# Kernel optimization log

Measured on AMD Instinct MI355X. Metric: run time of the kernel, lower is better.

Reference implementation:

```python
import jax, jax.numpy as jnp
import numpy as np

D_MOD = 256; H = 8; DH = 32; L_MAX = 96; NUM_MODULES = 15; NUM_TASKS = 7; LN_EPS = 1e-5


def _ln(x, s, b):
    mu = x.mean(-1, keepdims=True)
    v = ((x - mu) ** 2).mean(-1, keepdims=True)
    return (x - mu) * jax.lax.rsqrt(v + LN_EPS) * s + b


def _mha(x, w, b, key_mask, bias):
    # w: [4, D, D] (q,k,v,o), b: [4, D]
    B_, S, _ = x.shape
    q = (x @ w[0] + b[0]).reshape(B_, S, H, DH)
    k = (x @ w[1] + b[1]).reshape(B_, S, H, DH)
    v = (x @ w[2] + b[2]).reshape(B_, S, H, DH)
    logits = jnp.einsum('bihd,bjhd->bhij', q, k) / np.sqrt(DH).astype(np.float32)
    if bias is not None:
        logits = logits + bias
    if key_mask is not None:
        logits = jnp.where(key_mask[:, None, None, :], -1e9, logits)
    a = jax.nn.softmax(logits, axis=-1)
    o = jnp.einsum('bhij,bjhd->bihd', a, v).reshape(B_, S, D_MOD)
    return o @ w[3] + b[3]


def setup_inputs() -> dict:
    key = jax.random.key(0)
    ks = iter(jax.random.split(key, 48))
    B = 64
    M = B * NUM_MODULES  # 960 modules
    lengths = (16 + (np.arange(M) % 81)).astype(np.int32)  # ragged, max 96
    N = int(lengths.sum())  # 53346
    batch_ids = jnp.asarray(np.repeat(np.arange(M), lengths), jnp.int32)
    feats = jax.random.normal(next(ks), (N, D_MOD), jnp.float32)
    coords = jax.random.uniform(next(ks), (N, 3), jnp.float32) * 10.0
    module_to_event = jnp.asarray(np.arange(M) // NUM_MODULES, jnp.int32)
    module_pos = jnp.asarray(np.arange(M) % NUM_MODULES, jnp.int32)
    x_glob = jax.random.normal(next(ks), (B, 16), jnp.float32)

    def nrm(shape):
        return jax.random.normal(next(ks), shape, jnp.float32) * 0.02

    params = dict(
        cls_mod=nrm((1, 1, D_MOD)),
        empty_mod_emb=nrm((D_MOD,)),
        cls_task=nrm((1, NUM_TASKS, D_MOD)),
        pos_emb_table=nrm((1 + NUM_MODULES, D_MOD)),
        mod_attn_w=nrm((2, 4, D_MOD, D_MOD)), mod_attn_b=jnp.zeros((2, 4, D_MOD)),
        mod_rel=nrm((2, H, 3)),
        mod_ln_s=jnp.ones((2, 2, D_MOD)), mod_ln_b=jnp.zeros((2, 2, D_MOD)),
        mod_ffn_w1=nrm((2, D_MOD, 4 * D_MOD)), mod_ffn_b1=jnp.zeros((2, 4 * D_MOD)),
        mod_ffn_w2=nrm((2, 4 * D_MOD, D_MOD)), mod_ffn_b2=jnp.zeros((2, D_MOD)),
        glob_w1=nrm((16, D_MOD)), glob_b1=jnp.zeros((D_MOD,)),
        glob_w2=nrm((D_MOD, D_MOD)), glob_b2=jnp.zeros((D_MOD,)),
        evt_attn_w=nrm((3, 4, D_MOD, D_MOD)), evt_attn_b=jnp.zeros((3, 4, D_MOD)),
        evt_ln_s=jnp.ones((3, 2, D_MOD)), evt_ln_b=jnp.zeros((3, 2, D_MOD)),
        evt_ffn_w1=nrm((3, D_MOD, 2048)), evt_ffn_b1=jnp.zeros((3, 2048)),
        evt_ffn_w2=nrm((3, 2048, D_MOD)), evt_ffn_b2=jnp.zeros((3, D_MOD)),
        head_w=nrm((D_MOD, 16)), head_b=jnp.zeros((16,)),
    )
    return dict(feats=feats, coords=coords, batch_ids=batch_ids,
                module_to_event=module_to_event, module_pos=module_pos,
                x_glob=x_glob, **params)


def reference(feats, coords, batch_ids, module_to_event, module_pos, x_glob,
              cls_mod, empty_mod_emb, cls_task, pos_emb_table,
              mod_attn_w, mod_attn_b, mod_rel, mod_ln_s, mod_ln_b,
              mod_ffn_w1, mod_ffn_b1, mod_ffn_w2, mod_ffn_b2,
              glob_w1, glob_b1, glob_w2, glob_b2,
              evt_attn_w, evt_attn_b, evt_ln_s, evt_ln_b,
              evt_ffn_w1, evt_ffn_b1, evt_ffn_w2, evt_ffn_b2,
              head_w, head_b):
    M = module_to_event.shape[0]
    N = feats.shape[0]
    B = x_glob.shape[0]
    # --- ragged group/pad (pad_sequence over per-module masks) ---
    counts = jax.ops.segment_sum(jnp.ones((N,), jnp.int32), batch_ids, num_segments=M)
    starts = jnp.cumsum(counts) - counts
    pos = jnp.arange(N, dtype=jnp.int32) - starts[batch_ids]  # within-module rank (batch_ids sorted)
    pf = jnp.zeros((M, L_MAX, D_MOD), feats.dtype).at[batch_ids, pos].set(feats)
    pc = jnp.zeros((M, L_MAX, 3), coords.dtype).at[batch_ids, pos].set(coords)
    pad_mask = jnp.arange(L_MAX)[None, :] >= counts[:, None]
    # --- module transformer with relative-position bias, CLS token prepended ---
    seq = jnp.concatenate([jnp.broadcast_to(cls_mod, (M, 1, D_MOD)), pf], axis=1)  # [M,97,256]
    km = jnp.concatenate([jnp.zeros((M, 1), bool), pad_mask], axis=1)
    sc = jnp.concatenate([jnp.zeros((M, 1, 3), coords.dtype), pc], axis=1)
    rel = sc[:, :, None, :] - sc[:, None, :, :]  # [M,S,S,3]
    for l in range(2):
        bias = jnp.einsum('mijc,hc->mhij', rel, mod_rel[l])
        seq = _ln(seq + _mha(seq, mod_attn_w[l], mod_attn_b[l], km, bias), mod_ln_s[l, 0], mod_ln_b[l, 0])
        ff = jax.nn.gelu(seq @ mod_ffn_w1[l] + mod_ffn_b1[l], approximate=False) @ mod_ffn_w2[l] + mod_ffn_b2[l]
        seq = _ln(seq + ff, mod_ln_s[l, 1], mod_ln_b[l, 1])
    mod_emb = seq[:, 0]  # [M,256]
    # --- scatter-assembly into dense per-event tensor ---
    pad_evt = jnp.tile(empty_mod_emb[None, None, :], (B, NUM_MODULES, 1))
    pad_evt = pad_evt.at[module_to_event, module_pos].set(mod_emb)
    glob = (jax.nn.gelu(x_glob @ glob_w1 + glob_b1, approximate=False) @ glob_w2 + glob_b2)[:, None, :]
    se = jnp.concatenate([jnp.broadcast_to(cls_task, (B, NUM_TASKS, D_MOD)), glob, pad_evt], axis=1)  # [B,23,256]
    se = se.at[:, NUM_TASKS:].add(pos_emb_table[None])
    # --- event transformer (post-norm, ReLU FFN d_ff=2048, 3 layers) ---
    for l in range(3):
        se = _ln(se + _mha(se, evt_attn_w[l], evt_attn_b[l], None, None), evt_ln_s[l, 0], evt_ln_b[l, 0])
        ff = jax.nn.relu(se @ evt_ffn_w1[l] + evt_ffn_b1[l]) @ evt_ffn_w2[l] + evt_ffn_b2[l]
        se = _ln(se + ff, evt_ln_s[l, 1], evt_ln_b[l, 1])
    emb = se[:, :NUM_TASKS]

    def head(tok, sl):
        return emb[:, tok] @ head_w[:, sl] + head_b[sl]

    def norml(x):
        return x / jnp.maximum(jnp.linalg.norm(x, axis=-1, keepdims=True), 1e-12)

    sp = jax.nn.softplus
    # order: flavour(4), charm(1), e_vis_cc, e_vis_nc, pt_miss, lep_mag, lep_dir(3), jet_mag, jet_dir(3)
    # NOTE: original code's if/else overwrites flavour/charm with softplus too (replicated).
    out = jnp.concatenate([
        sp(head(0, slice(0, 4))), sp(head(1, slice(4, 5))), sp(head(2, slice(5, 6))),
        sp(head(3, slice(6, 7))), sp(head(4, slice(7, 8))), sp(head(5, slice(8, 9))),
        norml(head(5, slice(9, 12))), sp(head(6, slice(12, 13))), norml(head(6, slice(13, 16)))
    ], axis=-1)  # [B,16]
    return out
```

## Files before the change

### kernel.cpp

```cpp
#include <hip/hip_runtime.h>
#include <hip/hip_bf16.h>
#include <math.h>

typedef unsigned short u16;
typedef unsigned int u32;
typedef __bf16 bf16v8 __attribute__((ext_vector_type(8)));
typedef _Float16 f16v8 __attribute__((ext_vector_type(8)));
typedef __attribute__((ext_vector_type(4))) float f32x4;

#define D_MOD 256
#define NHEAD 8
#define DHEAD 32
#define SEQL 97
#define NTOKE 23

__device__ __forceinline__ float bf2f(u16 u){
  union { unsigned int i; float f; } x; x.i = ((unsigned int)u) << 16; return x.f;
}
__device__ __forceinline__ u16 f2bf(float f){
  return __builtin_bit_cast(u16, (__bf16)f);
}
__device__ __forceinline__ float gelu_fast(float v){
  float z = v * 0.70710678118654752f;
  float az = fabsf(z);
  float t = __builtin_amdgcn_rcpf(fmaf(0.3275911f, az, 1.0f));
  float p = t*(0.254829592f + t*(-0.284496736f + t*(1.421413741f + t*(-1.453152027f + t*1.061405429f))));
  float e = __expf(-z*z);
  float y = 1.0f - p*e;
  float erfz = copysignf(y, z);
  return 0.5f * v * (1.0f + erfz);
}
__device__ __forceinline__ void gld16(const void* g, void* l){
  __builtin_amdgcn_global_load_lds((const __attribute__((address_space(1))) void*)g,
                                   (__attribute__((address_space(3))) void*)l, 16, 0, 0);
}

__global__ __launch_bounds__(256) void prep_all(
    const float* __restrict__ aw, const float* __restrict__ ew,
    const float* __restrict__ f1m, const float* __restrict__ f2m,
    const float* __restrict__ f1e, const float* __restrict__ f2e,
    const float* __restrict__ gw2,
    u16* __restrict__ modWT, u16* __restrict__ evtWT,
    u16* __restrict__ modF1T, u16* __restrict__ modF2T,
    u16* __restrict__ evtF1T, u16* __restrict__ evtF2T,
    u16* __restrict__ globW2T,
    u16* __restrict__ WP, u16* __restrict__ F1P, u16* __restrict__ F2P)
{
  const int id = blockIdx.x;
  const float* src; u16* dst; u16* pk = nullptr; int K, N, kx, nx, t; long sS, dS;
  if (id < 512)      { t = id;        src = aw;  dst = modWT;   K=256;  N=256;  kx=8;  nx=8;  sS=65536;  dS=65536;  }
  else if (id < 1280){ t = id - 512;  src = ew;  dst = evtWT;   K=256;  N=256;  kx=8;  nx=8;  sS=65536;  dS=65536;  pk = WP;  }
  else if (id < 1792){ t = id - 1280; src = f1m; dst = modF1T;  K=256;  N=1024; kx=8;  nx=32; sS=262144; dS=262144; }
  else if (id < 2304){ t = id - 1792; src = f2m; dst = modF2T;  K=1024; N=256;  kx=32; nx=8;  sS=262144; dS=262144; }
  else if (id < 3840){ t = id - 2304; src = f1e; dst = evtF1T;  K=256;  N=2048; kx=8;  nx=64; sS=524288; dS=524288; pk = F1P; }
  else if (id < 5376){ t = id - 3840; src = f2e; dst = evtF2T;  K=2048; N=256;  kx=64; nx=8;  sS=524288; dS=524288; pk = F2P; }
  else               { t = id - 5376; src = gw2; dst = globW2T; K=256;  N=256;  kx=8;  nx=8;  sS=65536;  dS=65536;  }
  const int per = kx * nx;
  const int z = t / per, rem = t % per;
  const int k0 = (rem % kx) * 32, n0 = (rem / kx) * 32;
  src += (long)z * sS; dst += (long)z * dS;
  __shared__ float tt[32][33];
  const int tx = threadIdx.x & 31, ty = threadIdx.x >> 5;
  #pragma unroll
  for (int r = ty; r < 32; r += 8)
    tt[r][tx] = src[(long)(k0 + r) * N + n0 + tx];
  __syncthreads();
  #pragma unroll
  for (int r = ty; r < 32; r += 8)
    dst[(long)(n0 + r) * K + k0 + tx] = f2bf(tt[tx][r]);
  if (pk && threadIdx.x < 128){
    const int q = threadIdx.x >> 6, l = threadIdx.x & 63;
    const int nb = (n0 >> 4) + q, kb = k0 >> 5;
    const int c = q*16 + (l & 15);
    const int klb = (l >> 4) * 8;
    const long fragi = (long)nb * (K/32) + kb;
    u16 frag[8];
    #pragma unroll
    for (int e = 0; e < 8; e++) frag[e] = f2bf(tt[klb + e][c]);
    u16* d = pk + (long)z * (long)N * K + (fragi*64 + l)*8;
    *(uint4*)d = *(const uint4*)frag;
  }
}

__global__ void count_k(const int* __restrict__ bids, int* __restrict__ counts, int n){
  int i = blockIdx.x * blockDim.x + threadIdx.x;
  if (i < n) atomicAdd(&counts[bids[i]], 1);
}

__global__ void scan_k(const int* __restrict__ counts, int* __restrict__ starts, int M){
  __shared__ int buf[1024];
  int t = threadIdx.x;
  int v = (t < M) ? counts[t] : 0;
  buf[t] = v;
  __syncthreads();
  for (int o = 1; o < 1024; o <<= 1){
    int x = (t >= o) ? buf[t - o] : 0;
    __syncthreads();
    buf[t] += x;
    __syncthreads();
  }
  if (t < M) starts[t] = buf[t] - v;
}

__global__ __launch_bounds__(64) void cls_fill(u16* __restrict__ seqc, const float* __restrict__ cls_mod,
                                               const int* __restrict__ starts){
  int m = blockIdx.x, t = threadIdx.x;
  long row = (long)starts[m] + m;
  const float4 v = *(const float4*)(cls_mod + t * 4);
  u16* d = seqc + row * D_MOD + t * 4;
  d[0] = f2bf(v.x); d[1] = f2bf(v.y); d[2] = f2bf(v.z); d[3] = f2bf(v.w);
}

__global__ __launch_bounds__(64) void scatter_k(const float* __restrict__ feats, const float* __restrict__ coords,
                          const int* __restrict__ bids, u16* __restrict__ seqc, float* __restrict__ scc){
  int i = blockIdx.x, t = threadIdx.x;
  long row = (long)i + bids[i] + 1;
  const float4 v = *(const float4*)(feats + (long)i * D_MOD + t * 4);
  u16* d = seqc + row * D_MOD + t * 4;
  d[0] = f2bf(v.x); d[1] = f2bf(v.y); d[2] = f2bf(v.z); d[3] = f2bf(v.w);
  if (t < 3) scc[row * 3 + t] = coords[(long)i * 3 + t];
}

template<int EPI>
__global__ __launch_bounds__(512) void gemm256(
    const u16* __restrict__ A, const u16* __restrict__ Wt,
    const float* __restrict__ bias, const u16* __restrict__ resid,
    u16* __restrict__ C, int K, int N)
{
  __shared__ char smemraw[49152];
  u16* As = (u16*)smemraw;
  u16* Bs = (u16*)(smemraw + 32768);
  float* stg = (float*)smemraw;

  const int tid = threadIdx.x;
  const int w = tid >> 6, l = tid & 63;
  const int wr = w >> 1, wc = w & 1;

  const long nwg = (long)gridDim.x * gridDim.y;
  const long orig = (long)blockIdx.y * gridDim.x + blockIdx.x;
  const long q = nwg >> 3, r = nwg & 7;
  const long xcd = orig & 7, idx = orig >> 3;
  const long swz = (xcd < r ? xcd * (q + 1) : r * (q + 1) + (xcd - r) * q) + idx;
  const int colb = (int)(swz % gridDim.x);
  const long rowb = swz / gridDim.x;
  const long row0 = rowb * 256;
  const int col0 = colb * 128;

  const int fr = l & 15;
  const int ko = (l >> 4) * 8;
  f32x4 acc[4][4] = {};

  for (int kt = 0; kt < K; kt += 64){
    __syncthreads();
    #pragma unroll
    for (int p = 0; p < 4; p++){
      const int s = p * 512 + tid;
      const int inner = s & 1023, half = s >> 10;
      gld16(A + (row0 + (inner >> 2)) * K + kt + half*32 + (inner & 3)*8,
            As + (p*512 + w*64) * 8);
    }
    #pragma unroll
    for (int p = 0; p < 2; p++){
      const int s = p * 512 + tid;
      const int inner = s & 511, half = s >> 9;
      gld16(Wt + (long)(col0 + (inner >> 2)) * K + kt + half*32 + (inner & 3)*8,
            Bs + (p*512 + w*64) * 8);
    }
    __syncthreads();
    #pragma unroll
    for (int kk2 = 0; kk2 < 2; kk2++){
      bf16v8 af[4], bfv[4];
      #pragma unroll
      for (int mi = 0; mi < 4; mi++)
        af[mi] = __builtin_bit_cast(bf16v8, *(const uint4*)(As + kk2*8192 + (wr*64 + mi*16 + fr)*32 + ko));
      #pragma unroll
      for (int ni = 0; ni < 4; ni++)
        bfv[ni] = __builtin_bit_cast(bf16v8, *(const uint4*)(Bs + kk2*4096 + (wc*64 + ni*16 + fr)*32 + ko));
      #pragma unroll
      for (int mi = 0; mi < 4; mi++)
        #pragma unroll
        for (int ni = 0; ni < 4; ni++)
          acc[mi][ni] = __builtin_amdgcn_mfma_f32_16x16x32_bf16(af[mi], bfv[ni], acc[mi][ni], 0, 0, 0);
    }
  }

  const int rq = (l >> 4) * 4;
  #pragma unroll
  for (int p = 0; p < 8; p++){
    __syncthreads();
    if (wr == (p >> 1)){
      #pragma unroll
      for (int mm = 0; mm < 2; mm++){
        const int mi = (p & 1) * 2 + mm;
        #pragma unroll
        for (int ni = 0; ni < 4; ni++){
          const int coll = wc*64 + ni*16 + fr;
          const float bb = bias[col0 + coll];
          #pragma unroll
          for (int j = 0; j < 4; j++){
            float v = acc[mi][ni][j] + bb;
            if (EPI == 1) v = gelu_fast(v);
            if (EPI == 2) v = fmaxf(v, 0.0f);
            stg[(mm*16 + rq + j) * 132 + coll] = v;
          }
        }
      }
    }
    __syncthreads();
    {
      const int rowl = tid >> 4;
      const int cs = (tid & 15) * 8;
      const long gbase = (row0 + p*32 + rowl) * (long)N + col0 + cs;
      float4 lo = *(const float4*)(stg + rowl*132 + cs);
      float4 hi = *(const float4*)(stg + rowl*132 + cs + 4);
      float vv[8] = {lo.x, lo.y, lo.z, lo.w, hi.x, hi.y, hi.z, hi.w};
      if (EPI == 3){
        uint4 rv = *(const uint4*)(resid + gbase);
        const u16* rp = (const u16*)&rv;
        #pragma unroll
        for (int e = 0; e < 8; e++) vv[e] += bf2f(rp[e]);
      }
      uint4 ov;
      u16* op = (u16*)&ov;
      #pragma unroll
      for (int e = 0; e < 8; e++) op[e] = f2bf(vv[e]);
      *(uint4*)(C + gbase) = ov;
    }
  }
}

template<int NT>
__device__ __forceinline__ void attn_body(
    char* __restrict__ smemRaw,
    const u16* __restrict__ qkv, const float* __restrict__ scc,
    const float* __restrict__ rel, const int S, const long base,
    u16* __restrict__ out)
{
  constexpr int KS  = (NT + 1) / 2;
  constexpr int NK  = NT * 16;
  constexpr int STR = (KS * 32 <= 64) ? 64 : 128;
  constexpr int PBYTES = (NK * STR * 2 > NK * 132) ? NK * STR * 2 : NK * 132;
  u16* Pb = (u16*)smemRaw;
  u16* Vt = (u16*)(smemRaw + PBYTES);
  float* pj = (float*)(smemRaw + PBYTES + 32 * STR * 2);

  const int h = blockIdx.y;
  const int tid = threadIdx.x, w = tid >> 6, l = tid & 63;
  const int fr = l & 15, ko = (l >> 4) * 8;

  if (tid < NK){
    float v = 1e30f;
    if (tid < S){
      const float* s3 = scc + (base + tid) * 3;
      v = s3[0]*rel[h*3] + s3[1]*rel[h*3+1] + s3[2]*rel[h*3+2];
    }
    pj[tid] = v;
  }
  for (int idx = tid; idx < NK*32; idx += 256){
    int key = idx >> 5, d = idx & 31;
    float v = bf2f(qkv[(base + key)*768 + 512 + h*32 + d]);
    v = fminf(fmaxf(v, -60000.0f), 60000.0f);
    _Float16 hv = (_Float16)v;
    Vt[d*STR + (key ^ ((d & 7) << 3))] = __builtin_bit_cast(u16, hv);
  }
  for (int idx = tid; idx < 32*16; idx += 256){
    int d = idx >> 4, c = NK + (idx & 15);
    Vt[d*STR + (c ^ ((d & 7) << 3))] = 0;
  }
  for (int idx = tid; idx < NK*16; idx += 256){
    int row = idx >> 4, c = NK + (idx & 15);
    Pb[row*STR + (c ^ ((row & 7) << 3))] = 0;
  }
  __syncthreads();

  f32x4 accs[2][NT];
  bf16v8 kf[NT];
  #pragma unroll
  for (int nt = 0; nt < NT; nt++)
    kf[nt] = __builtin_bit_cast(bf16v8, *(const uint4*)(qkv + (base + nt*16 + fr)*768 + 256 + h*32 + ko));
  #pragma unroll
  for (int rr2 = 0; rr2 < 2; rr2++){
    const int rt = w + rr2*4;
    if (rt > NT - 1) break;
    bf16v8 qf = __builtin_bit_cast(bf16v8, *(const uint4*)(qkv + (base + rt*16 + fr)*768 + h*32 + ko));
    #pragma unroll
    for (int nt = 0; nt < NT; nt++){
      f32x4 z = {0.f, 0.f, 0.f, 0.f};
      accs[rr2][nt] = __builtin_amdgcn_mfma_f32_16x16x32_bf16(qf, kf[nt], z, 0, 0, 0);
    }
  }

  float pjr[NT];
  #pragma unroll
  for (int nt = 0; nt < NT; nt++) pjr[nt] = pj[nt*16 + fr];
  const float SCALE = 0.17677669529663687f;
  #pragma unroll
  for (int rr2 = 0; rr2 < 2; rr2++){
    const int rt = w + rr2*4;
    if (rt > NT - 1) break;
    #pragma unroll
    for (int j = 0; j < 4; j++){
      float x[NT], mx = -1e30f;
      #pragma unroll
      for (int nt = 0; nt < NT; nt++){
        x[nt] = accs[rr2][nt][j] * SCALE - pjr[nt];
        mx = fmaxf(mx, x[nt]);
      }
      #pragma unroll
      for (int o = 1; o < 16; o <<= 1) mx = fmaxf(mx, __shfl_xor(mx, o));
      float sum = 0.f;
      #pragma unroll
      for (int nt = 0; nt < NT; nt++){
        x[nt] = __expf(x[nt] - mx);
        sum += x[nt];
      }
      #pragma unroll
      for (int o = 1; o < 16; o <<= 1) sum += __shfl_xor(sum, o);
      const float inv = 1.0f / sum;
      const int row = rt*16 + (l >> 4)*4 + j;
      #pragma unroll
      for (int nt = 0; nt < NT; nt++){
        _Float16 hp = (_Float16)(x[nt] * inv);
        Pb[row*STR + ((nt*16 + fr) ^ ((row & 7) << 3))] = __builtin_bit_cast(u16, hp);
      }
    }
  }
  __syncthreads();

  f32x4 accO[2][2];
  #pragma unroll
  for (int rr2 = 0; rr2 < 2; rr2++){
    const int rt = w + rr2*4;
    if (rt > NT - 1) break;
    #pragma unroll
    for (int nt = 0; nt < 2; nt++){
      f32x4 z = {0.f, 0.f, 0.f, 0.f};
      accO[rr2][nt] = z;
    }
    #pragma unroll
    for (int ks = 0; ks < KS; ks++){
      const int prow = rt*16 + fr;
      f16v8 pa = __builtin_bit_cast(f16v8, *(const uint4*)(Pb + prow*STR + ((ks*32 + ko) ^ ((prow & 7) << 3))));
      #pragma unroll
      for (int nt = 0; nt < 2; nt++){
        const int vrow = nt*16 + fr;
        f16v8 vb = __builtin_bit_cast(f16v8, *(const uint4*)(Vt + vrow*STR + ((ks*32 + ko) ^ ((vrow & 7) << 3))));
        accO[rr2][nt] = __builtin_amdgcn_mfma_f32_16x16x32_f16(pa, vb, accO[rr2][nt], 0, 0, 0);
      }
    }
  }
  __syncthreads();

  float* O = (float*)smemRaw;
  #pragma unroll
  for (int rr2 = 0; rr2 < 2; rr2++){
    const int rt = w + rr2*4;
    if (rt > NT - 1) break;
    #pragma unroll
    for (int nt = 0; nt < 2; nt++)
      #pragma unroll
      for (int j = 0; j < 4; j++)
        O[(rt*16 + (l>>4)*4 + j)*33 + nt*16 + fr] = accO[rr2][nt][j];
  }
  __syncthreads();
  for (int idx = tid; idx < NK*16; idx += 256){
    const int row = idx >> 4;
    if (row >= S) continue;
    const int c = (idx & 15) * 2;
    const float f0 = O[row*33 + c], f1 = O[row*33 + c + 1];
    u32 pk = (u32)f2bf(f0) | ((u32)f2bf(f1) << 16);
    *(u32*)(out + (base + row)*256 + h*32 + c) = pk;
  }
}

__global__ __launch_bounds__(256) void mod_attn_all(
    const u16* __restrict__ qkv, const float* __restrict__ scc,
    const float* __restrict__ rel, const int* __restrict__ counts,
    const int* __restrict__ starts, u16* __restrict__ out)
{
  __shared__ __align__(16) char smem[37376];
  const int m = blockIdx.x;
  const int S = counts[m] + 1;
  const long base = (long)starts[m] + m;
  if (S <= 48)      attn_body<3>(smem, qkv, scc, rel, S, base, out);
  else if (S <= 80) attn_body<5>(smem, qkv, scc, rel, S, base, out);
  else              attn_body<7>(smem, qkv, scc, rel, S, base, out);
}

__global__ __launch_bounds__(256) void ln_k(u16* __restrict__ x, const float* __restrict__ s,
                                            const float* __restrict__ b, long nrows){
  const long row = (long)blockIdx.x * 4 + (threadIdx.x >> 6);
  if (row >= nrows) return;
  const int t = threadIdx.x & 63;
  u16* xr = x + row * D_MOD;
  uint2 rv = *(const uint2*)(xr + t * 4);
  float v0 = bf2f((u16)(rv.x & 0xffffu));
  float v1 = bf2f((u16)(rv.x >> 16));
  float v2 = bf2f((u16)(rv.y & 0xffffu));
  float v3 = bf2f((u16)(rv.y >> 16));
  float sum = v0 + v1 + v2 + v3;
  float sq  = v0*v0 + v1*v1 + v2*v2 + v3*v3;
  #pragma unroll
  for (int o = 32; o > 0; o >>= 1){
    sum += __shfl_xor(sum, o, 64);
    sq  += __shfl_xor(sq,  o, 64);
  }
  float mu = sum * (1.0f/256.0f);
  float var = sq * (1.0f/256.0f) - mu*mu;
  float rs = rsqrtf(var + 1e-5f);
  int c = t * 4;
  u16 o0 = f2bf((v0-mu)*rs*s[c+0]+b[c+0]);
  u16 o1 = f2bf((v1-mu)*rs*s[c+1]+b[c+1]);
  u16 o2 = f2bf((v2-mu)*rs*s[c+2]+b[c+2]);
  u16 o3 = f2bf((v3-mu)*rs*s[c+3]+b[c+3]);
  uint2 wv;
  wv.x = (unsigned)o0 | ((unsigned)o1 << 16);
  wv.y = (unsigned)o2 | ((unsigned)o3 << 16);
  *(uint2*)(xr + t * 4) = wv;
}

__global__ __launch_bounds__(512, 1) void evt_fused(
    u16* __restrict__ se,
    const u16* __restrict__ attnWP, const float* __restrict__ attnB,
    const u16* __restrict__ f1P, const float* __restrict__ f1B,
    const u16* __restrict__ f2P, const float* __restrict__ f2B,
    const float* __restrict__ lnS, const float* __restrict__ lnB)
{
  __shared__ u16 X[32*264];
  __shared__ u16 Yb[2*32*264];
  __shared__ u16 Sb[8*32*40];
  __shared__ float st1[32*8], st2[32*8];
  __shared__ float muA[32], rsA[32];

  const int b = blockIdx.x;
  const int tid = threadIdx.x, w = tid >> 6, l = tid & 63;
  const int fr = l & 15, hi4 = (l >> 4) * 4, ko = (l >> 4) * 8;
  const long tb = (long)b * NTOKE;
  u16* Sw = Sb + w * 1280;
  u16* Y = Yb;

  for (int idx = tid; idx < 736; idx += 512){
    const int row = idx >> 5, c8 = (idx & 31) * 8;
    *(uint4*)&X[row*264 + c8] = *(const uint4*)(se + (tb + row)*256 + c8);
  }
  for (int idx = tid; idx < 288; idx += 512){
    const int row = 23 + (idx >> 5), c8 = (idx & 31) * 8;
    uint4 z = {0,0,0,0};
    *(uint4*)&X[row*264 + c8] = z;
  }
  __syncthreads();

  for (int lay = 0; lay < 3; lay++){
    const u16*  WlP = attnWP + (long)lay * 4 * 65536;
    const float* Bl = attnB + lay * 1024;
    const u16*  F1  = f1P + (long)lay * 524288;
    const u16*  F2  = f2P + (long)lay * 524288;

    bf16v8 qf[2], kf[2], pa[2];
    {
      bf16v8 wr_[8][2];
      #pragma unroll
      for (int ks = 0; ks < 8; ks++)
        #pragma unroll
        for (int ct = 0; ct < 2; ct++)
          wr_[ks][ct] = __builtin_bit_cast(bf16v8, *(const uint4*)(WlP + ((w*2+ct)*8 + ks)*512 + l*8));
      f32x4 acc[2][2] = {};
      __builtin_amdgcn_s_setprio(1);
      #pragma unroll
      for (int ks = 0; ks < 8; ks++){
        bf16v8 a0 = __builtin_bit_cast(bf16v8, *(const uint4*)&X[fr*264 + ks*32 + ko]);
        bf16v8 a1 = __builtin_bit_cast(bf16v8, *(const uint4*)&X[(16+fr)*264 + ks*32 + ko]);
        #pragma unroll
        for (int ct = 0; ct < 2; ct++){
          acc[0][ct] = __builtin_amdgcn_mfma_f32_16x16x32_bf16(a0, wr_[ks][ct], acc[0][ct], 0, 0, 0);
          acc[1][ct] = __builtin_amdgcn_mfma_f32_16x16x32_bf16(a1, wr_[ks][ct], acc[1][ct], 0, 0, 0);
        }
      }
      __builtin_amdgcn_s_setprio(0);
      #pragma unroll
      for (int rt = 0; rt < 2; rt++)
        #pragma unroll
        for (int ct = 0; ct < 2; ct++){
          const float bb = Bl[w*32 + ct*16 + fr];
          #pragma unroll
          for (int j = 0; j < 4; j++)
            Sw[(rt*16 + hi4 + j)*40 + ct*16 + fr] = f2bf(acc[rt][ct][j] + bb);
        }
      qf[0] = __builtin_bit_cast(bf16v8, *(const uint4*)&Sw[fr*40 + ko]);
      qf[1] = __builtin_bit_cast(bf16v8, *(const uint4*)&Sw[(16+fr)*40 + ko]);
    }
    {
      bf16v8 wr_[8][2];
      #pragma unroll
      for (int ks = 0; ks < 8; ks++)
        #pragma unroll
        for (int ct = 0; ct < 2; ct++)
          wr_[ks][ct] = __builtin_bit_cast(bf16v8, *(const uint4*)(WlP + 65536 + ((w*2+ct)*8 + ks)*512 + l*8));
      f32x4 acc[2][2] = {};
      __builtin_amdgcn_s_setprio(1);
      #pragma unroll
      for (int ks = 0; ks < 8; ks++){
        bf16v8 a0 = __builtin_bit_cast(bf16v8, *(const uint4*)&X[fr*264 + ks*32 + ko]);
        bf16v8 a1 = __builtin_bit_cast(bf16v8, *(const uint4*)&X[(16+fr)*264 + ks*32 + ko]);
        #pragma unroll
        for (int ct = 0; ct < 2; ct++){
          acc[0][ct] = __builtin_amdgcn_mfma_f32_16x16x32_bf16(a0, wr_[ks][ct], acc[0][ct], 0, 0, 0);
          acc[1][ct] = __builtin_amdgcn_mfma_f32_16x16x32_bf16(a1, wr_[ks][ct], acc[1][ct], 0, 0, 0);
        }
      }
      __builtin_amdgcn_s_setprio(0);
      #pragma unroll
      for (int rt = 0; rt < 2; rt++)
        #pragma unroll
        for (int ct = 0; ct < 2; ct++){
          const float bb = Bl[256 + w*32 + ct*16 + fr];
          #pragma unroll
          for (int j = 0; j < 4; j++)
            Sw[(rt*16 + hi4 + j)*40 + ct*16 + fr] = f2bf(acc[rt][ct][j] + bb);
        }
      kf[0] = __builtin_bit_cast(bf16v8, *(const uint4*)&Sw[fr*40 + ko]);
      kf[1] = __builtin_bit_cast(bf16v8, *(const uint4*)&Sw[(16+fr)*40 + ko]);
    }
    {
      f32x4 accS[2][2];
      #pragma unroll
      for (int rt = 0; rt < 2; rt++)
        #pragma unroll
        for (int nt = 0; nt < 2; nt++){
          f32x4 z = {0.f,0.f,0.f,0.f};
          accS[rt][nt] = __builtin_amdgcn_mfma_f32_16x16x32_bf16(qf[rt], kf[nt], z, 0, 0, 0);
        }
      const float SCALE = 0.17677669529663687f;
      const bool v1 = (fr < 7);
      #pragma unroll
      for (int rt = 0; rt < 2; rt++){
        #pragma unroll
        for (int j = 0; j < 4; j++){
          float x0 = accS[rt][0][j] * SCALE;
          float x1 = v1 ? accS[rt][1][j] * SCALE : -1e30f;
          float mx = fmaxf(x0, x1);
          #pragma unroll
          for (int o = 1; o < 16; o <<= 1) mx = fmaxf(mx, __shfl_xor(mx, o));
          float e0 = __expf(x0 - mx);
          float e1 = v1 ? __expf(x1 - mx) : 0.0f;
          float sum = e0 + e1;
          #pragma unroll
          for (int o = 1; o < 16; o <<= 1) sum += __shfl_xor(sum, o);
          const float inv = 1.0f / sum;
          const int row = rt*16 + hi4 + j;
          Sw[row*40 + fr]      = f2bf(e0 * inv);
          Sw[row*40 + 16 + fr] = f2bf(e1 * inv);
        }
      }
      pa[0] = __builtin_bit_cast(bf16v8, *(const uint4*)&Sw[fr*40 + ko]);
      pa[1] = __builtin_bit_cast(bf16v8, *(const uint4*)&Sw[(16+fr)*40 + ko]);
    }
    {
      bf16v8 wr_[8][2];
      #pragma unroll
      for (int ks = 0; ks < 8; ks++)
        #pragma unroll
        for (int ct = 0; ct < 2; ct++)
          wr_[ks][ct] = __builtin_bit_cast(bf16v8, *(const uint4*)(WlP + 131072 + ((w*2+ct)*8 + ks)*512 + l*8));
      f32x4 acc[2][2] = {};
      __builtin_amdgcn_s_setprio(1);
      #pragma unroll
      for (int ks = 0; ks < 8; ks++){
        bf16v8 a0 = __builtin_bit_cast(bf16v8, *(const uint4*)&X[fr*264 + ks*32 + ko]);
        bf16v8 a1 = __builtin_bit_cast(bf16v8, *(const uint4*)&X[(16+fr)*264 + ks*32 + ko]);
        #pragma unroll
        for (int ct = 0; ct < 2; ct++){
          acc[0][ct] = __builtin_amdgcn_mfma_f32_16x16x32_bf16(a0, wr_[ks][ct], acc[0][ct], 0, 0, 0);
          acc[1][ct] = __builtin_amdgcn_mfma_f32_16x16x32_bf16(a1, wr_[ks][ct], acc[1][ct], 0, 0, 0);
        }
      }
      __builtin_amdgcn_s_setprio(0);
      #pragma unroll
      for (int rt = 0; rt < 2; rt++)
        #pragma unroll
        for (int ct = 0; ct < 2; ct++){
          const float bb = Bl[512 + w*32 + ct*16 + fr];
          u16* dst = &Sw[(ct*16 + fr)*40 + rt*16 + hi4];
          #pragma unroll
          for (int j = 0; j < 4; j++)
            dst[j] = f2bf(acc[rt][ct][j] + bb);
        }
      bf16v8 vb0 = __builtin_bit_cast(bf16v8, *(const uint4*)&Sw[fr*40 + ko]);
      bf16v8 vb1 = __builtin_bit_cast(bf16v8, *(const uint4*)&Sw[(16+fr)*40 + ko]);
      f32x4 accO[2][2];
      #pragma unroll
      for (int rt = 0; rt < 2; rt++){
        f32x4 z = {0.f,0.f,0.f,0.f};
        accO[rt][0] = __builtin_amdgcn_mfma_f32_16x16x32_bf16(pa[rt], vb0, z, 0, 0, 0);
        accO[rt][1] = __builtin_amdgcn_mfma_f32_16x16x32_bf16(pa[rt], vb1, z, 0, 0, 0);
      }
      #pragma unroll
      for (int rt = 0; rt < 2; rt++)
        #pragma unroll
        for (int nt = 0; nt < 2; nt++)
          #pragma unroll
          for (int j = 0; j < 4; j++)
            Y[(rt*16 + hi4 + j)*264 + w*32 + nt*16 + fr] = f2bf(accO[rt][nt][j]);
    }
    __syncthreads();

    {
      bf16v8 wr_[8][2];
      #pragma unroll
      for (int ks = 0; ks < 8; ks++)
        #pragma unroll
        for (int ct = 0; ct < 2; ct++)
          wr_[ks][ct] = __builtin_bit_cast(bf16v8, *(const uint4*)(WlP + 196608 + ((w*2+ct)*8 + ks)*512 + l*8));
      f32x4 acc[2][2] = {};
      __builtin_amdgcn_s_setprio(1);
      #pragma unroll
      for (int ks = 0; ks < 8; ks++){
        bf16v8 a0 = __builtin_bit_cast(bf16v8, *(const uint4*)&Y[fr*264 + ks*32 + ko]);
        bf16v8 a1 = __builtin_bit_cast(bf16v8, *(const uint4*)&Y[(16+fr)*264 + ks*32 + ko]);
        #pragma unroll
        for (int ct = 0; ct < 2; ct++){
          acc[0][ct] = __builtin_amdgcn_mfma_f32_16x16x32_bf16(a0, wr_[ks][ct], acc[0][ct], 0, 0, 0);
          acc[1][ct] = __builtin_amdgcn_mfma_f32_16x16x32_bf16(a1, wr_[ks][ct], acc[1][ct], 0, 0, 0);
        }
      }
      __builtin_amdgcn_s_setprio(0);
      float val[2][2][4];
      #pragma unroll
      for (int ct = 0; ct < 2; ct++){
        const int col = w*32 + ct*16 + fr;
        const float bb = Bl[768 + col];
        #pragma unroll
        for (int rt = 0; rt < 2; rt++)
          #pragma unroll
          for (int j = 0; j < 4; j++)
            val[rt][ct][j] = acc[rt][ct][j] + bb + bf2f(X[(rt*16 + hi4 + j)*264 + col]);
      }
      #pragma unroll
      for (int rt = 0; rt < 2; rt++)
        #pragma unroll
        for (int j = 0; j < 4; j++){
          float s1 = val[rt][0][j] + val[rt][1][j];
          float s2 = val[rt][0][j]*val[rt][0][j] + val[rt][1][j]*val[rt][1][j];
          #pragma unroll
          for (int o = 1; o < 16; o <<= 1){ s1 += __shfl_xor(s1, o); s2 += __shfl_xor(s2, o); }
          if (fr == 0){
            const int row = rt*16 + hi4 + j;
            st1[row*8 + w] = s1; st2[row*8 + w] = s2;
          }
        }
      __syncthreads();
      if (tid < 32){
        float s1 = 0.f, s2 = 0.f;
        #pragma unroll
        for (int k = 0; k < 8; k++){ s1 += st1[tid*8 + k]; s2 += st2[tid*8 + k]; }
        const float mu = s1 * (1.0f/256.0f);
        const float var = s2 * (1.0f/256.0f) - mu*mu;
        muA[tid] = mu; rsA[tid] = rsqrtf(var + 1e-5f);
      }
      __syncthreads();
      #pragma unroll
      for (int ct = 0; ct < 2; ct++){
        const int col = w*32 + ct*16 + fr;
        const float lw = lnS[lay*512 + col], lb = lnB[lay*512 + col];
        #pragma unroll
        for (int rt = 0; rt < 2; rt++)
          #pragma unroll
          for (int j = 0; j < 4; j++){
            const int row = rt*16 + hi4 + j;
            X[row*264 + col] = f2bf((val[rt][ct][j] - muA[row]) * rsA[row] * lw + lb);
          }
      }
      __syncthreads();
    }

    {
      f32x4 acc2[2][2] = {};
      for (int c = 0; c < 8; c++){
        u16* Yc = Yb + (c & 1) * 8448;
        bf16v8 w1r[8][2];
        #pragma unroll
        for (int ks = 0; ks < 8; ks++)
          #pragma unroll
          for (int ct = 0; ct < 2; ct++)
            w1r[ks][ct] = __builtin_bit_cast(bf16v8, *(const uint4*)(F1 + (long)((c*16 + w*2 + ct)*8 + ks)*512 + l*8));
        f32x4 acc1[2][2] = {};
        __builtin_amdgcn_s_setprio(1);
        #pragma unroll
        for (int ks = 0; ks < 8; ks++){
          bf16v8 a0 = __builtin_bit_cast(bf16v8, *(const uint4*)&X[fr*264 + ks*32 + ko]);
          bf16v8 a1 = __builtin_bit_cast(bf16v8, *(const uint4*)&X[(16+fr)*264 + ks*32 + ko]);
          #pragma unroll
          for (int ct = 0; ct < 2; ct++){
            acc1[0][ct] = __builtin_amdgcn_mfma_f32_16x16x32_bf16(a0, w1r[ks][ct], acc1[0][ct], 0, 0, 0);
            acc1[1][ct] = __builtin_amdgcn_mfma_f32_16x16x32_bf16(a1, w1r[ks][ct], acc1[1][ct], 0, 0, 0);
          }
        }
        __builtin_amdgcn_s_setprio(0);
        bf16v8 w2r[8][2];
        #pragma unroll
        for (int ks = 0; ks < 8; ks++)
          #pragma unroll
          for (int ct = 0; ct < 2; ct++)
            w2r[ks][ct] = __builtin_bit_cast(bf16v8, *(const uint4*)(F2 + (long)((w*2+ct)*64 + c*8 + ks)*512 + l*8));
        #pragma unroll
        for (int ct = 0; ct < 2; ct++){
          const float bb = f1B[lay*2048 + c*256 + w*32 + ct*16 + fr];
          #pragma unroll
          for (int rt = 0; rt < 2; rt++)
            #pragma unroll
            for (int j = 0; j < 4; j++)
              Yc[(rt*16 + hi4 + j)*264 + w*32 + ct*16 + fr] = f2bf(fmaxf(acc1[rt][ct][j] + bb, 0.0f));
        }
        __syncthreads();
        __builtin_amdgcn_s_setprio(1);
        #pragma unroll
        for (int ks = 0; ks < 8; ks++){
          bf16v8 a0 = __builtin_bit_cast(bf16v8, *(const uint4*)&Yc[fr*264 + ks*32 + ko]);
          bf16v8 a1 = __builtin_bit_cast(bf16v8, *(const uint4*)&Yc[(16+fr)*264 + ks*32 + ko]);
          #pragma unroll
          for (int ct = 0; ct < 2; ct++){
            acc2[0][ct] = __builtin_amdgcn_mfma_f32_16x16x32_bf16(a0, w2r[ks][ct], acc2[0][ct], 0, 0, 0);
            acc2[1][ct] = __builtin_amdgcn_mfma_f32_16x16x32_bf16(a1, w2r[ks][ct], acc2[1][ct], 0, 0, 0);
          }
        }
        __builtin_amdgcn_s_setprio(0);
      }
      __syncthreads();
      float val[2][2][4];
      #pragma unroll
      for (int ct = 0; ct < 2; ct++){
        const int col = w*32 + ct*16 + fr;
        const float bb = f2B[lay*256 + col];
        #pragma unroll
        for (int rt = 0; rt < 2; rt++)
          #pragma unroll
          for (int j = 0; j < 4; j++)
            val[rt][ct][j] = acc2[rt][ct][j] + bb + bf2f(X[(rt*16 + hi4 + j)*264 + col]);
      }
      #pragma unroll
      for (int rt = 0; rt < 2; rt++)
        #pragma unroll
        for (int j = 0; j < 4; j++){
          float s1 = val[rt][0][j] + val[rt][1][j];
          float s2 = val[rt][0][j]*val[rt][0][j] + val[rt][1][j]*val[rt][1][j];
          #pragma unroll
          for (int o = 1; o < 16; o <<= 1){ s1 += __shfl_xor(s1, o); s2 += __shfl_xor(s2, o); }
          if (fr == 0){
            const int row = rt*16 + hi4 + j;
            st1[row*8 + w] = s1; st2[row*8 + w] = s2;
          }
        }
      __syncthreads();
      if (tid < 32){
        float s1 = 0.f, s2 = 0.f;
        #pragma unroll
        for (int k = 0; k < 8; k++){ s1 += st1[tid*8 + k]; s2 += st2[tid*8 + k]; }
        const float mu = s1 * (1.0f/256.0f);
        const float var = s2 * (1.0f/256.0f) - mu*mu;
        muA[tid] = mu; rsA[tid] = rsqrtf(var + 1e-5f);
      }
      __syncthreads();
      #pragma unroll
      for (int ct = 0; ct < 2; ct++){
        const int col = w*32 + ct*16 + fr;
        const float lw = lnS[lay*512 + 256 + col], lb = lnB[lay*512 + 256 + col];
        #pragma unroll
        for (int rt = 0; rt < 2; rt++)
          #pragma unroll
          for (int j = 0; j < 4; j++){
            const int row = rt*16 + hi4 + j;
            X[row*264 + col] = f2bf((val[rt][ct][j] - muA[row]) * rsA[row] * lw + lb);
          }
      }
      __syncthreads();
    }
  }

  for (int idx = tid; idx < 736; idx += 512){
    const int row = idx >> 5, c8 = (idx & 31) * 8;
    *(uint4*)(se + (tb + row)*256 + c8) = *(const uint4*)&X[row*264 + c8];
  }
}

__global__ __launch_bounds__(256) void glob1_k(const float* __restrict__ xg, const float* __restrict__ w1,
                                               const float* __restrict__ b1, u16* __restrict__ h){
  int b = blockIdx.x, d = threadIdx.x;
  float s = b1[d];
  #pragma unroll
  for (int k = 0; k < 16; k++) s += xg[b*16 + k] * w1[k*256 + d];
  h[(long)b*256 + d] = f2bf(gelu_fast(s));
}

__global__ __launch_bounds__(64) void fill_se(u16* __restrict__ se, const float* __restrict__ cls_task,
                                              const u16* __restrict__ globo, const float* __restrict__ pos_emb,
                                              const float* __restrict__ empty_emb){
  int bt = blockIdx.x;
  int b = bt / NTOKE, tk = bt % NTOKE;
  int t = threadIdx.x;
  u16* d = se + (long)bt * D_MOD;
  #pragma unroll
  for (int j = 0; j < 4; j++){
    int c = t*4 + j;
    float v;
    if (tk < 7) v = cls_task[tk*D_MOD + c];
    else if (tk == 7) v = bf2f(globo[(long)b*D_MOD + c]) + pos_emb[c];
    else v = empty_emb[c] + pos_emb[(tk - 7)*D_MOD + c];
    d[c] = f2bf(v);
  }
}

__global__ __launch_bounds__(64) void scatter_mod(u16* __restrict__ se, const u16* __restrict__ seqc,
                                                  const int* __restrict__ m2e, const int* __restrict__ mpos,
                                                  const int* __restrict__ starts,
                                                  const float* __restrict__ pos_emb){
  int m = blockIdx.x, t = threadIdx.x;
  int e = m2e[m], p = mpos[m];
  const u16* src = seqc + ((long)starts[m] + m) * D_MOD;
  u16* dst = se + ((long)e * NTOKE + 8 + p) * D_MOD;
  const float* pe = pos_emb + (long)(1 + p) * D_MOD;
  #pragma unroll
  for (int j = 0; j < 4; j++){
    int c = t*4 + j;
    dst[c] = f2bf(bf2f(src[c]) + pe[c]);
  }
}

__global__ __launch_bounds__(64) void heads_k(const u16* __restrict__ se, const float* __restrict__ hw,
                                              const float* __restrict__ hb, float* __restrict__ out){
  int b = blockIdx.x, t = threadIdx.x;
  __shared__ float raw[16];
  if (t < 16){
    int tok = (t < 4) ? 0 : (t <= 8) ? (t - 3) : (t <= 11) ? 5 : 6;
    const u16* e = se + ((long)b * NTOKE + tok) * D_MOD;
    float s = hb[t];
    for (int d = 0; d < 256; d++) s += bf2f(e[d]) * hw[d*16 + t];
    raw[t] = s;
  }
  __syncthreads();
  if (t < 16){
    float v = raw[t];
    float r;
    if (t <= 8 || t == 12){
      r = fmaxf(v, 0.0f) + log1pf(__expf(-fabsf(v)));
    } else if (t <= 11){
      float n = sqrtf(raw[9]*raw[9] + raw[10]*raw[10] + raw[11]*raw[11]);
      r = v / fmaxf(n, 1e-12f);
    } else {
      float n = sqrtf(raw[13]*raw[13] + raw[14]*raw[14] + raw[15]*raw[15]);
      r = v / fmaxf(n, 1e-12f);
    }
    out[b*16 + t] = r;
  }
}

extern "C" void kernel_launch(void* const* d_in, const int* in_sizes, int n_in,
                              void* d_out, int out_size, void* d_ws, size_t ws_size,
                              hipStream_t stream){
  const float* feats      = (const float*)d_in[0];
  const float* coords     = (const float*)d_in[1];
  const int*   batch_ids  = (const int*)d_in[2];
  const int*   m2e        = (const int*)d_in[3];
  const int*   mpos       = (const int*)d_in[4];
  const float* x_glob     = (const float*)d_in[5];
  const float* cls_mod    = (const float*)d_in[6];
  const float* empty_emb  = (const float*)d_in[7];
  const float* cls_task   = (const float*)d_in[8];
  const float* pos_emb    = (const float*)d_in[9];
  const float* mod_attn_w = (const float*)d_in[10];
  const float* mod_attn_b = (const float*)d_in[11];
  const float* mod_rel    = (const float*)d_in[12];
  const float* mod_ln_s   = (const float*)d_in[13];
  const float* mod_ln_b   = (const float*)d_in[14];
  const float* mod_ffn_w1 = (const float*)d_in[15];
  const float* mod_ffn_b1 = (const float*)d_in[16];
  const float* mod_ffn_w2 = (const float*)d_in[17];
  const float* mod_ffn_b2 = (const float*)d_in[18];
  const float* glob_w1    = (const float*)d_in[19];
  const float* glob_b1    = (const float*)d_in[20];
  const float* glob_w2    = (const float*)d_in[21];
  const float* glob_b2    = (const float*)d_in[22];
  const float* evt_attn_w = (const float*)d_in[23];
  const float* evt_attn_b = (const float*)d_in[24];
  const float* evt_ln_s   = (const float*)d_in[25];
  const float* evt_ln_b   = (const float*)d_in[26];
  const float* evt_ffn_w1 = (const float*)d_in[27];
  const float* evt_ffn_b1 = (const float*)d_in[28];
  const float* evt_ffn_w2 = (const float*)d_in[29];
  const float* evt_ffn_b2 = (const float*)d_in[30];
  const float* head_w     = (const float*)d_in[31];
  const float* head_b     = (const float*)d_in[32];
  float* out = (float*)d_out;

  const int N = in_sizes[0] / 256;
  const int M = in_sizes[3];
  const int B = in_sizes[5] / 16;
  const long CROWS   = (long)M + N;
  const long CROWS_P = (((CROWS + 255) >> 8) << 8) + 256;
  const long TE  = (long)B * NTOKE;

  char* ws = (char*)d_ws;
  u16* modWT   = (u16*)ws;
  u16* evtWT   = modWT + 8L*65536;
  u16* modF1T  = evtWT + 12L*65536;
  u16* modF2T  = modF1T + 2L*262144;
  u16* evtF1T  = modF2T + 2L*262144;
  u16* evtF2T  = evtF1T + 3L*524288;
  u16* globW2T = evtF2T + 3L*524288;
  size_t off = 11468800;
  int* counts = (int*)(ws + off); off += 16*1024;
  int* starts = (int*)(ws + off); off += 16*1024;
  float* scc  = (float*)(ws + off); off += ((size_t)CROWS_P*12 + 255) & ~(size_t)255;
  u16* seqc   = (u16*)(ws + off); off += (size_t)CROWS_P * D_MOD * 2;
  off = (off + 255) & ~(size_t)255;
  const size_t OFF_BIG = off;
  u16* qkv   = (u16*)(ws + OFF_BIG);
  u16* attno = (u16*)(ws + OFF_BIG + (size_t)CROWS_P*768*2);
  u16* ffh   = (u16*)(ws + OFF_BIG);
  u16* se    = (u16*)(ws + OFF_BIG);
  u16* globh = (u16*)(ws + OFF_BIG + 12*1024*1024);
  u16* globo = (u16*)(ws + OFF_BIG + 13*1024*1024);
  u16* evtWP  = (u16*)(ws + OFF_BIG + 120L*1024*1024);
  u16* evtF1P = evtWP + 12L*65536;
  u16* evtF2P = evtF1P + 3L*524288;

  prep_all<<<5440, 256, 0, stream>>>(mod_attn_w, evt_attn_w, mod_ffn_w1, mod_ffn_w2,
                                     evt_ffn_w1, evt_ffn_w2, glob_w2,
                                     modWT, evtWT, modF1T, modF2T, evtF1T, evtF2T, globW2T,
                                     evtWP, evtF1P, evtF2P);

  hipMemsetAsync(counts, 0, (size_t)M*4, stream);
  hipMemsetAsync(scc, 0, (size_t)CROWS_P*12, stream);
  hipMemsetAsync(seqc + CROWS*D_MOD, 0, (size_t)(CROWS_P - CROWS)*D_MOD*2, stream);
  count_k<<<(N + 255)/256, 256, 0, stream>>>(batch_ids, counts, N);
  scan_k<<<1, 1024, 0, stream>>>(counts, starts, M);
  cls_fill<<<M, 64, 0, stream>>>(seqc, cls_mod, starts);
  scatter_k<<<N, 64, 0, stream>>>(feats, coords, batch_ids, seqc, scc);

  const int RB = (int)(CROWS_P / 256);
  for (int l = 0; l < 2; l++){
    gemm256<0><<<dim3(6, RB), 512, 0, stream>>>(seqc, modWT + (long)l*4*65536,
        mod_attn_b + l*1024, nullptr, qkv, 256, 768);
    mod_attn_all<<<dim3(M, NHEAD), 256, 0, stream>>>(qkv, scc, mod_rel + l*24, counts, starts, attno);
    gemm256<3><<<dim3(2, RB), 512, 0, stream>>>(attno, modWT + ((long)l*4+3)*65536,
        mod_attn_b + l*1024 + 768, seqc, seqc, 256, 256);
    ln_k<<<(int)((CROWS + 3)/4), 256, 0, stream>>>(seqc, mod_ln_s + (l*2)*256, mod_ln_b + (l*2)*256, CROWS);
    gemm256<1><<<dim3(8, RB), 512, 0, stream>>>(seqc, modF1T + (long)l*262144,
        mod_ffn_b1 + l*1024, nullptr, ffh, 256, 1024);
    gemm256<3><<<dim3(2, RB), 512, 0, stream>>>(ffh, modF2T + (long)l*262144,
        mod_ffn_b2 + l*256, seqc, seqc, 1024, 256);
    ln_k<<<(int)((CROWS + 3)/4), 256, 0, stream>>>(seqc, mod_ln_s + (l*2+1)*256, mod_ln_b + (l*2+1)*256, CROWS);
  }

  hipMemsetAsync(globh, 0, 256*256*2, stream);
  glob1_k<<<B, 256, 0, stream>>>(x_glob, glob_w1, glob_b1, globh);
  gemm256<0><<<dim3(2, 1), 512, 0, stream>>>(globh, globW2T, glob_b2, nullptr, globo, 256, 256);
  fill_se<<<(int)TE, 64, 0, stream>>>(se, cls_task, globo, pos_emb, empty_emb);
  scatter_mod<<<M, 64, 0, stream>>>(se, seqc, m2e, mpos, starts, pos_emb);

  evt_fused<<<B, 512, 0, stream>>>(se, evtWP, evt_attn_b, evtF1P, evt_ffn_b1,
                                   evtF2P, evt_ffn_b2, evt_ln_s, evt_ln_b);

  heads_k<<<B, 64, 0, stream>>>(se, head_w, head_b, out);
}
```

Before: 825.1 us.

## Fuse residual add and LayerNorm into full-width output GEMM for module layers

Adds a gemm_ln kernel in which each block computes all 256 output columns for 128 rows, adds bias and residual, and applies LayerNorm in the epilogue. It replaces the gemm256<3> plus separate ln_k pair after attention and after the FFN in both module layers. This removes four LayerNorm launches and one read-modify-write of the sequence buffer per fusion. The cost is fewer, larger blocks (RB2 blocks along rows, one along columns), which may reduce parallelism. Padding rows of attno are now zeroed as well.

```diff
diff --git a/kernel.cpp b/kernel.cpp
--- a/kernel.cpp
+++ b/kernel.cpp
@@ -229,6 +229,123 @@
   }
 }
 
+__global__ __launch_bounds__(512) void gemm_ln(
+    const u16* __restrict__ A, const u16* __restrict__ Wt,
+    const float* __restrict__ bias, const u16* __restrict__ resid,
+    u16* __restrict__ C, int K,
+    const float* __restrict__ lnS, const float* __restrict__ lnB)
+{
+  __shared__ char smemraw[49152];
+  u16* As = (u16*)smemraw;
+  u16* Bs = (u16*)(smemraw + 16384);
+  float* stg = (float*)smemraw;
+
+  const int tid = threadIdx.x;
+  const int w = tid >> 6, l = tid & 63;
+  const int wr = w >> 2, wc = w & 3;
+
+  const long nwg = gridDim.y;
+  const long orig = blockIdx.y;
+  const long q = nwg >> 3, r = nwg & 7;
+  const long xcd = orig & 7, idx = orig >> 3;
+  const long swz = (xcd < r ? xcd * (q + 1) : r * (q + 1) + (xcd - r) * q) + idx;
+  const long row0 = swz * 128;
+
+  const int fr = l & 15;
+  const int ko = (l >> 4) * 8;
+  f32x4 acc[4][4] = {};
+
+  for (int kt = 0; kt < K; kt += 64){
+    __syncthreads();
+    #pragma unroll
+    for (int p = 0; p < 2; p++){
+      const int s = p * 512 + tid;
+      const int inner = s & 511, half = s >> 9;
+      gld16(A + (row0 + (inner >> 2)) * K + kt + half*32 + (inner & 3)*8,
+            As + (p*512 + w*64) * 8);
+    }
+    #pragma unroll
+    for (int p = 0; p < 4; p++){
+      const int s = p * 512 + tid;
+      const int inner = s & 1023, half = s >> 10;
+      gld16(Wt + (long)(inner >> 2) * K + kt + half*32 + (inner & 3)*8,
+            Bs + (p*512 + w*64) * 8);
+    }
+    __syncthreads();
+    #pragma unroll
+    for (int kk2 = 0; kk2 < 2; kk2++){
+      bf16v8 af[4], bfv[4];
+      #pragma unroll
+      for (int mi = 0; mi < 4; mi++)
+        af[mi] = __builtin_bit_cast(bf16v8, *(const uint4*)(As + kk2*4096 + (wr*64 + mi*16 + fr)*32 + ko));
+      #pragma unroll
+      for (int ni = 0; ni < 4; ni++)
+        bfv[ni] = __builtin_bit_cast(bf16v8, *(const uint4*)(Bs + kk2*8192 + (wc*64 + ni*16 + fr)*32 + ko));
+      #pragma unroll
+      for (int mi = 0; mi < 4; mi++)
+        #pragma unroll
+        for (int ni = 0; ni < 4; ni++)
+          acc[mi][ni] = __builtin_amdgcn_mfma_f32_16x16x32_bf16(af[mi], bfv[ni], acc[mi][ni], 0, 0, 0);
+    }
+  }
+
+  const int rq = (l >> 4) * 4;
+  #pragma unroll
+  for (int p = 0; p < 4; p++){
+    __syncthreads();
+    if (wr == (p >> 1)){
+      #pragma unroll
+      for (int mm = 0; mm < 2; mm++){
+        const int mi = (p & 1) * 2 + mm;
+        #pragma unroll
+        for (int ni = 0; ni < 4; ni++){
+          const int coll = wc*64 + ni*16 + fr;
+          const float bb = bias[coll];
+          #pragma unroll
+          for (int j = 0; j < 4; j++)
+            stg[(mm*16 + rq + j) * 260 + coll] = acc[mi][ni][j] + bb;
+        }
+      }
+    }
+    __syncthreads();
+    {
+      const int rowl = tid >> 4;
+      const int c0 = (tid & 15) * 16;
+      const long gbase = (row0 + p*32 + rowl) * 256 + c0;
+      float v[16];
+      uint4 r0 = *(const uint4*)(resid + gbase);
+      uint4 r1 = *(const uint4*)(resid + gbase + 8);
+      const u16* rp0 = (const u16*)&r0;
+      const u16* rp1 = (const u16*)&r1;
+      #pragma unroll
+      for (int e = 0; e < 8; e++){
+        v[e]     = stg[rowl*260 + c0 + e]     + bf2f(rp0[e]);
+        v[8 + e] = stg[rowl*260 + c0 + 8 + e] + bf2f(rp1[e]);
+      }
+      float sum = 0.f, sq = 0.f;
+      #pragma unroll
+      for (int e = 0; e < 16; e++){ sum += v[e]; sq += v[e]*v[e]; }
+      #pragma unroll
+      for (int o = 1; o < 16; o <<= 1){
+        sum += __shfl_xor(sum, o);
+        sq  += __shfl_xor(sq,  o);
+      }
+      const float mu = sum * (1.0f/256.0f);
+      const float var = sq * (1.0f/256.0f) - mu*mu;
+      const float rs = rsqrtf(var + 1e-5f);
+      uint4 o0, o1;
+      u16* op0 = (u16*)&o0; u16* op1 = (u16*)&o1;
+      #pragma unroll
+      for (int e = 0; e < 8; e++){
+        op0[e] = f2bf((v[e]     - mu) * rs * lnS[c0 + e]     + lnB[c0 + e]);
+        op1[e] = f2bf((v[8 + e] - mu) * rs * lnS[c0 + 8 + e] + lnB[c0 + 8 + e]);
+      }
+      *(uint4*)(C + gbase)     = o0;
+      *(uint4*)(C + gbase + 8) = o1;
+    }
+  }
+}
+
 template<int NT>
 __device__ __forceinline__ void attn_body(
     char* __restrict__ smemRaw,
@@ -385,38 +502,6 @@
   if (S <= 48)      attn_body<3>(smem, qkv, scc, rel, S, base, out);
   else if (S <= 80) attn_body<5>(smem, qkv, scc, rel, S, base, out);
   else              attn_body<7>(smem, qkv, scc, rel, S, base, out);
-}
-
-__global__ __launch_bounds__(256) void ln_k(u16* __restrict__ x, const float* __restrict__ s,
-                                            const float* __restrict__ b, long nrows){
-  const long row = (long)blockIdx.x * 4 + (threadIdx.x >> 6);
-  if (row >= nrows) return;
-  const int t = threadIdx.x & 63;
-  u16* xr = x + row * D_MOD;
-  uint2 rv = *(const uint2*)(xr + t * 4);
-  float v0 = bf2f((u16)(rv.x & 0xffffu));
-  float v1 = bf2f((u16)(rv.x >> 16));
-  float v2 = bf2f((u16)(rv.y & 0xffffu));
-  float v3 = bf2f((u16)(rv.y >> 16));
-  float sum = v0 + v1 + v2 + v3;
-  float sq  = v0*v0 + v1*v1 + v2*v2 + v3*v3;
-  #pragma unroll
-  for (int o = 32; o > 0; o >>= 1){
-    sum += __shfl_xor(sum, o, 64);
-    sq  += __shfl_xor(sq,  o, 64);
-  }
-  float mu = sum * (1.0f/256.0f);
-  float var = sq * (1.0f/256.0f) - mu*mu;
-  float rs = rsqrtf(var + 1e-5f);
-  int c = t * 4;
-  u16 o0 = f2bf((v0-mu)*rs*s[c+0]+b[c+0]);
-  u16 o1 = f2bf((v1-mu)*rs*s[c+1]+b[c+1]);
-  u16 o2 = f2bf((v2-mu)*rs*s[c+2]+b[c+2]);
-  u16 o3 = f2bf((v3-mu)*rs*s[c+3]+b[c+3]);
-  uint2 wv;
-  wv.x = (unsigned)o0 | ((unsigned)o1 << 16);
-  wv.y = (unsigned)o2 | ((unsigned)o3 << 16);
-  *(uint2*)(xr + t * 4) = wv;
 }
 
 __global__ __launch_bounds__(512, 1) void evt_fused(
@@ -931,24 +1016,26 @@
   hipMemsetAsync(counts, 0, (size_t)M*4, stream);
   hipMemsetAsync(scc, 0, (size_t)CROWS_P*12, stream);
   hipMemsetAsync(seqc + CROWS*D_MOD, 0, (size_t)(CROWS_P - CROWS)*D_MOD*2, stream);
+  hipMemsetAsync(attno + CROWS*D_MOD, 0, (size_t)(CROWS_P - CROWS)*D_MOD*2, stream);
   count_k<<<(N + 255)/256, 256, 0, stream>>>(batch_ids, counts, N);
   scan_k<<<1, 1024, 0, stream>>>(counts, starts, M);
   cls_fill<<<M, 64, 0, stream>>>(seqc, cls_mod, starts);
   scatter_k<<<N, 64, 0, stream>>>(feats, coords, batch_ids, seqc, scc);
 
   const int RB = (int)(CROWS_P / 256);
+  const int RB2 = (int)(CROWS_P / 128);
   for (int l = 0; l < 2; l++){
     gemm256<0><<<dim3(6, RB), 512, 0, stream>>>(seqc, modWT + (long)l*4*65536,
         mod_attn_b + l*1024, nullptr, qkv, 256, 768);
     mod_attn_all<<<dim3(M, NHEAD), 256, 0, stream>>>(qkv, scc, mod_rel + l*24, counts, starts, attno);
-    gemm256<3><<<dim3(2, RB), 512, 0, stream>>>(attno, modWT + ((long)l*4+3)*65536,
-        mod_attn_b + l*1024 + 768, seqc, seqc, 256, 256);
-    ln_k<<<(int)((CROWS + 3)/4), 256, 0, stream>>>(seqc, mod_ln_s + (l*2)*256, mod_ln_b + (l*2)*256, CROWS);
+    gemm_ln<<<dim3(1, RB2), 512, 0, stream>>>(attno, modWT + ((long)l*4+3)*65536,
+        mod_attn_b + l*1024 + 768, seqc, seqc, 256,
+        mod_ln_s + (l*2)*256, mod_ln_b + (l*2)*256);
     gemm256<1><<<dim3(8, RB), 512, 0, stream>>>(seqc, modF1T + (long)l*262144,
         mod_ffn_b1 + l*1024, nullptr, ffh, 256, 1024);
-    gemm256<3><<<dim3(2, RB), 512, 0, stream>>>(ffh, modF2T + (long)l*262144,
-        mod_ffn_b2 + l*256, seqc, seqc, 1024, 256);
-    ln_k<<<(int)((CROWS + 3)/4), 256, 0, stream>>>(seqc, mod_ln_s + (l*2+1)*256, mod_ln_b + (l*2+1)*256, CROWS);
+    gemm_ln<<<dim3(1, RB2), 512, 0, stream>>>(ffh, modF2T + (long)l*262144,
+        mod_ffn_b2 + l*256, seqc, seqc, 1024,
+        mod_ln_s + (l*2+1)*256, mod_ln_b + (l*2+1)*256);
   }
 
   hipMemsetAsync(globh, 0, 256*256*2, stream);
```

Result: slower. 852.6 us (+3.3%).

## Triple-buffer LDS in gemm256 with async prefetch of next K-slice

Applied to the files above, without the earlier changes.

Restructures the gemm256 main loop from a synchronous 64-wide K tile with two barriers per step into a three-buffer pipeline of 32-wide K slices. The next slice is issued with async global-to-LDS loads, followed by a partial vmcnt wait and a single barrier per step. The goal is to hide global load latency behind MFMA work. In exchange LDS grows to 72KB, which may lower occupancy, and the loop now runs twice as many iterations, each with less MFMA work between barriers.

```diff
diff --git a/kernel.cpp b/kernel.cpp
--- a/kernel.cpp
+++ b/kernel.cpp
@@ -127,9 +127,7 @@
     const float* __restrict__ bias, const u16* __restrict__ resid,
     u16* __restrict__ C, int K, int N)
 {
-  __shared__ char smemraw[49152];
-  u16* As = (u16*)smemraw;
-  u16* Bs = (u16*)(smemraw + 32768);
+  __shared__ __align__(16) char smemraw[73728];
   float* stg = (float*)smemraw;
 
   const int tid = threadIdx.x;
@@ -150,38 +148,55 @@
   const int ko = (l >> 4) * 8;
   f32x4 acc[4][4] = {};
 
-  for (int kt = 0; kt < K; kt += 64){
-    __syncthreads();
+  const int sA1 = 512 + tid;
+  const long arow0 = row0 + (tid >> 2), arow1 = row0 + (sA1 >> 2);
+  const int ac0 = (tid & 3) * 8, ac1 = (sA1 & 3) * 8;
+  const long brow = col0 + (tid >> 2);
+  const int bc0 = (tid & 3) * 8;
+  const int ldsA0 = (0*512 + w*64) * 8;
+  const int ldsA1 = (1*512 + w*64) * 8;
+  const int ldsB0 = (w*64) * 8;
+
+  const int NH = K >> 5;
+
+  {
+    u16* bufA = (u16*)smemraw;
+    u16* bufB = (u16*)(smemraw + 16384);
+    gld16(A  + arow0 * K + ac0, bufA + ldsA0);
+    gld16(A  + arow1 * K + ac1, bufA + ldsA1);
+    gld16(Wt + brow  * K + bc0, bufB + ldsB0);
+  }
+
+  int cb = 0, nb = 1;
+  for (int h = 0; h < NH; h++){
+    if (h + 1 < NH){
+      const int kc = (h + 1) * 32;
+      u16* bufA = (u16*)(smemraw + nb * 24576);
+      u16* bufB = (u16*)(smemraw + nb * 24576 + 16384);
+      gld16(A  + arow0 * K + kc + ac0, bufA + ldsA0);
+      gld16(A  + arow1 * K + kc + ac1, bufA + ldsA1);
+      gld16(Wt + brow  * K + kc + bc0, bufB + ldsB0);
+      asm volatile("s_waitcnt vmcnt(3)" ::: "memory");
+    } else {
+      asm volatile("s_waitcnt vmcnt(0)" ::: "memory");
+    }
+    __builtin_amdgcn_s_barrier();
+    __builtin_amdgcn_sched_barrier(0);
+    const u16* cA = (const u16*)(smemraw + cb * 24576);
+    const u16* cB = (const u16*)(smemraw + cb * 24576 + 16384);
+    bf16v8 af[4], bfv[4];
     #pragma unroll
-    for (int p = 0; p < 4; p++){
-      const int s = p * 512 + tid;
-      const int inner = s & 1023, half = s >> 10;
-      gld16(A + (row0 + (inner >> 2)) * K + kt + half*32 + (inner & 3)*8,
-            As + (p*512 + w*64) * 8);
-    }
+    for (int mi = 0; mi < 4; mi++)
+      af[mi] = __builtin_bit_cast(bf16v8, *(const uint4*)(cA + (wr*64 + mi*16 + fr)*32 + ko));
     #pragma unroll
-    for (int p = 0; p < 2; p++){
-      const int s = p * 512 + tid;
-      const int inner = s & 511, half = s >> 9;
-      gld16(Wt + (long)(col0 + (inner >> 2)) * K + kt + half*32 + (inner & 3)*8,
-            Bs + (p*512 + w*64) * 8);
-    }
-    __syncthreads();
+    for (int ni = 0; ni < 4; ni++)
+      bfv[ni] = __builtin_bit_cast(bf16v8, *(const uint4*)(cB + (wc*64 + ni*16 + fr)*32 + ko));
     #pragma unroll
-    for (int kk2 = 0; kk2 < 2; kk2++){
-      bf16v8 af[4], bfv[4];
-      #pragma unroll
-      for (int mi = 0; mi < 4; mi++)
-        af[mi] = __builtin_bit_cast(bf16v8, *(const uint4*)(As + kk2*8192 + (wr*64 + mi*16 + fr)*32 + ko));
+    for (int mi = 0; mi < 4; mi++)
       #pragma unroll
       for (int ni = 0; ni < 4; ni++)
-        bfv[ni] = __builtin_bit_cast(bf16v8, *(const uint4*)(Bs + kk2*4096 + (wc*64 + ni*16 + fr)*32 + ko));
-      #pragma unroll
-      for (int mi = 0; mi < 4; mi++)
-        #pragma unroll
-        for (int ni = 0; ni < 4; ni++)
-          acc[mi][ni] = __builtin_amdgcn_mfma_f32_16x16x32_bf16(af[mi], bfv[ni], acc[mi][ni], 0, 0, 0);
-    }
+        acc[mi][ni] = __builtin_amdgcn_mfma_f32_16x16x32_bf16(af[mi], bfv[ni], acc[mi][ni], 0, 0, 0);
+    cb = nb; nb = (nb == 2) ? 0 : nb + 1;
   }
 
   const int rq = (l >> 4) * 4;
```

New measurement: 809.3 us. About the same (-1.9%).
